# Kernel tuning notes

Measured on AMD Instinct MI355X. Metric: run time of the kernel, lower is better.

Reference implementation:

```python
import jax, jax.numpy as jnp
import numpy as np

B, F, U, H1, H2 = 2048, 256, 64, 64, 32
E = F + 1  # attention embed dim = num_inputs + 1


def setup_inputs() -> dict:
    key = jax.random.key(0)
    ks = jax.random.split(key, 14)
    s = lambda fan: 1.0 / np.sqrt(fan)
    inp = {
        "x": jax.random.normal(ks[0], (B, F), jnp.float32),
        # stacked per-feature FeatureNN params (Linear(1,U) -> Linear(U,H1) -> Linear(H1,H2) -> Linear(H2,1))
        "w1": jax.random.normal(ks[1], (F, U), jnp.float32) * s(1),
        "b1": jnp.zeros((F, U), jnp.float32),
        "w2": jax.random.normal(ks[2], (F, U, H1), jnp.float32) * s(U),
        "b2": jnp.zeros((F, H1), jnp.float32),
        "w3": jax.random.normal(ks[3], (F, H1, H2), jnp.float32) * s(H1),
        "b3": jnp.zeros((F, H2), jnp.float32),
        "w4": jax.random.normal(ks[4], (F, H2), jnp.float32) * s(H2),
        "b4": jnp.zeros((F,), jnp.float32),
        # MultiheadAttention(E, 1) params: packed qkv in_proj + out_proj
        "in_w": jax.random.normal(ks[5], (3 * E, E), jnp.float32) * s(E),
        "in_b": jnp.zeros((3 * E,), jnp.float32),
        "out_w": jax.random.normal(ks[6], (E, E), jnp.float32) * s(E),
        "out_b": jnp.zeros((E,), jnp.float32),
        "bias": jnp.zeros((1,), jnp.float32),
    }
    return inp


def _attention(x, in_w, in_b, out_w, out_b):
    # x: [B, F]; build [B, F, E] = concat(one-hot feature index, value)
    b = x.shape[0]
    eye = jnp.eye(F, dtype=x.dtype)
    xa = jnp.concatenate([jnp.broadcast_to(eye, (b, F, F)), x[:, :, None]], axis=-1)  # [B,F,E]
    qkv = jnp.einsum("bse,fe->bsf", xa, in_w) + in_b  # [B,F,3E]
    q, k, v = jnp.split(qkv, 3, axis=-1)
    scores = jnp.einsum("bqe,bke->bqk", q, k) / jnp.sqrt(jnp.asarray(E, x.dtype))
    attn = jax.nn.softmax(scores, axis=-1)
    ctx = jnp.einsum("bqk,bke->bqe", attn, v)
    out = jnp.einsum("bqe,fe->bqf", ctx, out_w) + out_b  # out_proj
    return out[:, :, -1]  # keep only the value channel -> [B, F]


def _feature_nns(x, w1, b1, w2, b2, w3, b3, w4, b4):
    # x: [B, F] -> per-feature independent MLPs, batched across features
    h = jax.nn.relu(x[:, :, None] * w1[None] + b1[None])          # [B,F,U]
    h = jax.nn.relu(jnp.einsum("bfu,fuh->bfh", h, w2) + b2[None])  # [B,F,H1]
    h = jax.nn.relu(jnp.einsum("bfh,fhg->bfg", h, w3) + b3[None])  # [B,F,H2]
    return jnp.einsum("bfg,fg->bf", h, w4) + b4[None]              # [B,F]


def reference(x, w1, b1, w2, b2, w3, b3, w4, b4, in_w, in_b, out_w, out_b, bias):
    xa = _attention(x, in_w, in_b, out_w, out_b)                   # att_before_flag=True
    fo = _feature_nns(xa, w1, b1, w2, b2, w3, b3, w4, b4)          # dropout is identity (p=0 / eval)
    out = jnp.sum(fo, axis=-1) + bias                              # [B] + bias -> [B]
    return (out, fo)
```

## Files before the change

### kernel.cpp

```cpp
#include <hip/hip_runtime.h>

#define BB 2048
#define FF 256
#define EE 257
#define UU 64
#define HH1 64
#define HH2 32

#define SC 0.089992807f

typedef __attribute__((ext_vector_type(8))) short short8;
typedef __attribute__((ext_vector_type(4))) float f32x4;
typedef __attribute__((ext_vector_type(4))) unsigned u32x4;
typedef __attribute__((ext_vector_type(2))) unsigned u32x2;

#define MF(a, b, c) __builtin_amdgcn_mfma_f32_16x16x32_bf16(a, b, c, 0, 0, 0)
#define EXP2(x) __builtin_amdgcn_exp2f(x)

__device__ inline unsigned cvt_pk(float a, float b) {
    unsigned r;
    asm("v_cvt_pk_bf16_f32 %0, %1, %2" : "=v"(r) : "v"(a), "v"(b));
    return r;
}
struct HiLo { unsigned hi, lo; };
__device__ inline HiLo split2(float a, float b) {
    HiLo r;
    r.hi = cvt_pk(a, b);
    float ha = __builtin_bit_cast(float, r.hi << 16);
    float hb = __builtin_bit_cast(float, r.hi & 0xFFFF0000u);
    r.lo = cvt_pk(a - ha, b - hb);
    return r;
}

__global__ __launch_bounds__(256) void k_prep(const float* __restrict__ in_w,
                                              const float* __restrict__ in_b,
                                              const float* __restrict__ out_w,
                                              const float* __restrict__ out_b,
                                              const float* __restrict__ w2,
                                              const float* __restrict__ w3,
                                              float* __restrict__ mt,
                                              float* __restrict__ uv, float* __restrict__ wgf,
                                              float* __restrict__ sc,
                                              short* __restrict__ w2s, short* __restrict__ w3s) {
    const int blk = blockIdx.x;
    const int t = threadIdx.x;
    __shared__ float red[4][256];
    __shared__ float s0[EE + 3];
    __shared__ float s1[EE + 3];
    if (blk < 256) {
        const int ki = blk;
        for (int j = t; j < EE; j += 256) {
            s0[j] = in_w[(EE + j) * EE + ki] + in_b[EE + j];
            s1[j] = in_b[j];
        }
        __syncthreads();
        const int w = t >> 6, l = t & 63;
        const int j0 = (w * EE) >> 2, j1 = ((w + 1) * EE) >> 2;
        float acc[4] = {0.f, 0.f, 0.f, 0.f};
#pragma unroll 4
        for (int j = j0; j < j1; ++j) {
            float ak = s0[j];
            float bj = s1[j];
#pragma unroll
            for (int g = 0; g < 4; ++g) {
                float aq = in_w[j * EE + l + 64 * g] + bj;
                acc[g] = fmaf(aq, ak, acc[g]);
            }
        }
#pragma unroll
        for (int g = 0; g < 4; ++g) red[w][l + 64 * g] = acc[g];
        __syncthreads();
        {
            float s = red[0][t] + red[1][t] + red[2][t] + red[3][t];
            mt[(ki >> 1) * 512 + t * 2 + (ki & 1)] = s * SC;
        }
    } else if (blk < 512) {
        const int f = blk - 256;
        const int l = t & 63, q = t >> 6;
        const int lr = l & 15, lq = l >> 4;
        const float* w2f = w2 + f * (UU * HH1);
        const float* w3f = w3 + f * (HH1 * HH2);
        short* o2 = w2s + f * 8192;
        short* o3 = w3s + f * 4096;
        const int hperm = (q & 1) * 32 + (lr >> 2) * 8 + ((q >> 1) << 2) + (lr & 3);
#pragma unroll
        for (int kb = 0; kb < 2; ++kb) {
            float v[8];
#pragma unroll
            for (int j = 0; j < 8; ++j) v[j] = w2f[(kb * 32 + lq * 8 + j) * HH1 + hperm];
            u32x4 hi, lo;
#pragma unroll
            for (int p = 0; p < 4; ++p) {
                HiLo s = split2(v[2 * p], v[2 * p + 1]);
                hi[p] = s.hi; lo[p] = s.lo;
            }
            *(short8*)(o2 + ((0 * 2 + kb) * 4 + q) * 512 + l * 8) = __builtin_bit_cast(short8, hi);
            *(short8*)(o2 + ((1 * 2 + kb) * 4 + q) * 512 + l * 8) = __builtin_bit_cast(short8, lo);
        }
        {
            const int kb = q & 1, ct = q >> 1;
            float v[8];
#pragma unroll
            for (int j = 0; j < 8; ++j) v[j] = w3f[(kb * 32 + lq * 8 + j) * HH2 + ct * 16 + lr];
            u32x4 hi, lo;
#pragma unroll
            for (int p = 0; p < 4; ++p) {
                HiLo s = split2(v[2 * p], v[2 * p + 1]);
                hi[p] = s.hi; lo[p] = s.lo;
            }
            *(short8*)(o3 + ((0 * 2 + kb) * 2 + ct) * 512 + l * 8) = __builtin_bit_cast(short8, hi);
            *(short8*)(o3 + ((1 * 2 + kb) * 2 + ct) * 512 + l * 8) = __builtin_bit_cast(short8, lo);
        }
    } else if (blk < 515) {
        const int which = blk - 512;
        for (int j = t; j < EE; j += 256) {
            if (which == 0)      { s0[j] = in_w[(EE + j) * EE + FF];    s1[j] = in_b[j]; }
            else if (which == 1) { s0[j] = in_w[j * EE + FF];           s1[j] = in_b[EE + j]; }
            else                 { s0[j] = out_w[(EE - 1) * EE + j];    s1[j] = in_b[2 * EE + j]; }
        }
        __syncthreads();
        const int w = t >> 6, l = t & 63;
        const int j0 = (w * EE) >> 2, j1 = ((w + 1) * EE) >> 2;
        const int rowbase = which * EE;
        float acc[4] = {0.f, 0.f, 0.f, 0.f};
#pragma unroll 4
        for (int j = j0; j < j1; ++j) {
            float sk = s0[j];
            float bj = s1[j];
#pragma unroll
            for (int g = 0; g < 4; ++g) {
                float av = in_w[(rowbase + j) * EE + l + 64 * g] + bj;
                acc[g] = fmaf(av, sk, acc[g]);
            }
        }
#pragma unroll
        for (int g = 0; g < 4; ++g) red[w][l + 64 * g] = acc[g];
        __syncthreads();
        {
            float s = red[0][t] + red[1][t] + red[2][t] + red[3][t];
            if (which == 0)      uv[t]          = s * SC;
            else if (which == 1) wgf[2 * t]     = s * SC;
            else                 wgf[2 * t + 1] = s;
        }
    } else {
        const int j = t;
        float cq = in_w[j * EE + FF];
        float ck = in_w[(EE + j) * EE + FF];
        float cv = in_w[(2 * EE + j) * EE + FF];
        float rj = out_w[(EE - 1) * EE + j];
        float pa = cq * ck, pb = cv * rj;
        if (t == 0) {
            const int j2 = 256;
            pa += in_w[j2 * EE + FF] * in_w[(EE + j2) * EE + FF];
            pb += in_w[(2 * EE + j2) * EE + FF] * out_w[(EE - 1) * EE + j2];
        }
#pragma unroll
        for (int o = 32; o > 0; o >>= 1) {
            pa += __shfl_down(pa, o, 64);
            pb += __shfl_down(pb, o, 64);
        }
        if ((t & 63) == 0) { red[0][t >> 6] = pa; red[1][t >> 6] = pb; }
        __syncthreads();
        if (t == 0) {
            pa = red[0][0] + red[0][1] + red[0][2] + red[0][3];
            pb = red[1][0] + red[1][1] + red[1][2] + red[1][3];
            sc[0] = pa * SC;
            sc[1] = pb;
            sc[2] = out_b[EE - 1];
        }
    }
}

__global__ __launch_bounds__(256) void k2_attn(const float* __restrict__ x,
                                               const float2* __restrict__ mt2,
                                               const float* __restrict__ uv,
                                               const float* __restrict__ wg,
                                               const float* __restrict__ sc,
                                               float* __restrict__ xa) {
    const int qi = threadIdx.x;
    const int b0 = blockIdx.x * 2;
    __shared__ __align__(16) float xs0[FF];
    __shared__ __align__(16) float xs1[FF];
    __shared__ __align__(16) float wgs[2 * FF];
    xs0[qi] = x[b0 * FF + qi];
    xs1[qi] = x[(b0 + 1) * FF + qi];
    *(float2*)&wgs[2 * qi] = *(const float2*)&wg[2 * qi];
    const float alpha_s = sc[0], beta = sc[1], ob = sc[2];
    const float uq = uv[qi];
    __syncthreads();
    const float xq0 = xs0[qi];
    const float xq1 = xs1[qi];
    const float a0 = fmaf(alpha_s, xq0, uq);
    const float a1 = fmaf(alpha_s, xq1, uq);
    float le0 = 0.f, le1 = 0.f, p0 = 0.f, p1 = 0.f, q0 = 0.f, q1 = 0.f;
#pragma unroll 8
    for (int kp = 0; kp < FF / 2; ++kp) {
        const float2 m   = mt2[kp * FF + qi];
        const f32x4 wgk  = *(const f32x4*)&wgs[4 * kp];
        const float2 xk0 = *(const float2*)&xs0[2 * kp];
        const float2 xk1 = *(const float2*)&xs1[2 * kp];
        float e;
        e = EXP2(fmaf(xk0.x, a0, fmaf(wgk[0], xq0, m.x))); le0 += e; p0 = fmaf(e, wgk[1], p0); q0 = fmaf(e, xk0.x, q0);
        e = EXP2(fmaf(xk0.y, a0, fmaf(wgk[2], xq0, m.y))); le0 += e; p0 = fmaf(e, wgk[3], p0); q0 = fmaf(e, xk0.y, q0);
        e = EXP2(fmaf(xk1.x, a1, fmaf(wgk[0], xq1, m.x))); le1 += e; p1 = fmaf(e, wgk[1], p1); q1 = fmaf(e, xk1.x, q1);
        e = EXP2(fmaf(xk1.y, a1, fmaf(wgk[2], xq1, m.y))); le1 += e; p1 = fmaf(e, wgk[3], p1); q1 = fmaf(e, xk1.y, q1);
    }
    xa[b0 * FF + qi]       = (p0 + beta * q0) / le0 + ob;
    xa[(b0 + 1) * FF + qi] = (p1 + beta * q1) / le1 + ob;
}

__global__ __launch_bounds__(256, 3) void k3_fnn(const float* xa_in,
                                                 const float* __restrict__ w1,
                                                 const float* __restrict__ b1,
                                                 const float* __restrict__ b2,
                                                 const float* __restrict__ b3,
                                                 const float* __restrict__ w4,
                                                 const float* __restrict__ b4,
                                                 const short* __restrict__ w2s,
                                                 const short* __restrict__ w3s,
                                                 float* fo) {
    const int fidx = blockIdx.x & 255;
    const int f   = ((fidx & 7) << 5) | (fidx >> 3);
    const int rq  = blockIdx.x >> 8;
    const int tid = threadIdx.x;
    const int wv  = tid >> 6;
    const int l   = tid & 63;
    const int lr  = l & 15;
    const int lq  = l >> 4;

    const float* w1f = w1 + f * UU;
    const float* b1f = b1 + f * UU;
    const float* b2f = b2 + f * HH1;
    const float* b3f = b3 + f * HH2;
    const float* w4f = w4 + f * HH2;
    const short* w2sf = w2s + f * 8192;
    const short* w3sf = w3s + f * 4096;
    const float b4v  = b4[f];

    short8 W3h[2][2], W3l[2][2];
#pragma unroll
    for (int ct = 0; ct < 2; ++ct)
#pragma unroll
        for (int kb = 0; kb < 2; ++kb) {
            W3h[ct][kb] = *(const short8*)(w3sf + ((0 * 2 + kb) * 2 + ct) * 512 + l * 8);
            W3l[ct][kb] = *(const short8*)(w3sf + ((1 * 2 + kb) * 2 + ct) * 512 + l * 8);
        }
    f32x4 B3v[2], W4v[2];
#pragma unroll
    for (int ct = 0; ct < 2; ++ct) {
        B3v[ct] = *(const f32x4*)(b3f + ct * 16 + lq * 4);
        W4v[ct] = *(const f32x4*)(w4f + ct * 16 + lq * 4);
    }

    __shared__ __align__(16) short w2l[8192];
#pragma unroll
    for (int i = 0; i < 4; ++i)
        *(short8*)(w2l + (tid * 4 + i) * 8) = *(const short8*)(w2sf + (tid * 4 + i) * 8);
    __syncthreads();

    const int cstart = (rq * 64) / 3;
    const int cend   = ((rq + 1) * 64) / 3;
    int ch = cstart + wv;
    if (ch >= cend) return;
    float xv0 = xa_in[(ch * 32 + lr) * FF + f];
    float xv1 = xa_in[(ch * 32 + 16 + lr) * FF + f];
    for (; ch < cend; ch += 4) {
        const int rows0 = ch * 32;
        float nxv0 = 0.f, nxv1 = 0.f;
        if (ch + 4 < cend) {
            nxv0 = xa_in[((ch + 4) * 32 + lr) * FF + f];
            nxv1 = xa_in[((ch + 4) * 32 + 16 + lr) * FF + f];
        }

        short8 Bh[2][2], Bl[2][2];
#pragma unroll
        for (int kb = 0; kb < 2; ++kb) {
            f32x4 wA = *(const f32x4*)(w1f + kb * 32 + lq * 8);
            f32x4 wB = *(const f32x4*)(w1f + kb * 32 + lq * 8 + 4);
            f32x4 bA = *(const f32x4*)(b1f + kb * 32 + lq * 8);
            f32x4 bB = *(const f32x4*)(b1f + kb * 32 + lq * 8 + 4);
#pragma unroll
            for (int rbt = 0; rbt < 2; ++rbt) {
                const float xv = rbt ? xv1 : xv0;
                float h[8];
#pragma unroll
                for (int j = 0; j < 4; ++j) h[j]     = fmaxf(fmaf(xv, wA[j], bA[j]), 0.f);
#pragma unroll
                for (int j = 0; j < 4; ++j) h[4 + j] = fmaxf(fmaf(xv, wB[j], bB[j]), 0.f);
                u32x4 bh, bl;
#pragma unroll
                for (int p = 0; p < 4; ++p) {
                    HiLo s = split2(h[2 * p], h[2 * p + 1]);
                    bh[p] = s.hi; bl[p] = s.lo;
                }
                Bh[rbt][kb] = __builtin_bit_cast(short8, bh);
                Bl[rbt][kb] = __builtin_bit_cast(short8, bl);
            }
        }

        f32x4 acc[2][4];
#pragma unroll
        for (int ht = 0; ht < 4; ++ht) {
            const short8 W2h0 = *(const short8*)(w2l + (0 * 4 + ht) * 512 + l * 8);
            const short8 W2h1 = *(const short8*)(w2l + (1 * 4 + ht) * 512 + l * 8);
            const short8 W2l0 = *(const short8*)(w2l + (2 * 4 + ht) * 512 + l * 8);
            const short8 W2l1 = *(const short8*)(w2l + (3 * 4 + ht) * 512 + l * 8);
            const f32x4 binit = *(const f32x4*)(b2f + (ht & 1) * 32 + lq * 8 + ((ht >> 1) << 2));
#pragma unroll
            for (int rbt = 0; rbt < 2; ++rbt) {
                f32x4 a = binit;
                a = MF(W2h0, Bh[rbt][0], a);
                a = MF(W2h1, Bh[rbt][1], a);
                a = MF(W2h0, Bl[rbt][0], a);
                a = MF(W2h1, Bl[rbt][1], a);
                a = MF(W2l0, Bh[rbt][0], a);
                a = MF(W2l1, Bh[rbt][1], a);
                acc[rbt][ht] = a;
            }
        }

#pragma unroll
        for (int rbt = 0; rbt < 2; ++rbt) {
            short8 Bh3[2], Bl3[2];
#pragma unroll
            for (int kb = 0; kb < 2; ++kb) {
                float e0 = fmaxf(acc[rbt][kb][0], 0.f),     e1 = fmaxf(acc[rbt][kb][1], 0.f);
                float e2 = fmaxf(acc[rbt][kb][2], 0.f),     e3 = fmaxf(acc[rbt][kb][3], 0.f);
                float e4 = fmaxf(acc[rbt][kb + 2][0], 0.f), e5 = fmaxf(acc[rbt][kb + 2][1], 0.f);
                float e6 = fmaxf(acc[rbt][kb + 2][2], 0.f), e7 = fmaxf(acc[rbt][kb + 2][3], 0.f);
                HiLo p0 = split2(e0, e1), p1 = split2(e2, e3);
                HiLo p2 = split2(e4, e5), p3 = split2(e6, e7);
                u32x4 bh, bl;
                bh[0] = p0.hi; bh[1] = p1.hi; bh[2] = p2.hi; bh[3] = p3.hi;
                bl[0] = p0.lo; bl[1] = p1.lo; bl[2] = p2.lo; bl[3] = p3.lo;
                Bh3[kb] = __builtin_bit_cast(short8, bh);
                Bl3[kb] = __builtin_bit_cast(short8, bl);
            }
            float part = 0.f;
#pragma unroll
            for (int ct = 0; ct < 2; ++ct) {
                f32x4 a2 = B3v[ct];
                a2 = MF(W3h[ct][0], Bh3[0], a2);
                a2 = MF(W3h[ct][1], Bh3[1], a2);
                a2 = MF(W3h[ct][0], Bl3[0], a2);
                a2 = MF(W3h[ct][1], Bl3[1], a2);
                a2 = MF(W3l[ct][0], Bh3[0], a2);
                a2 = MF(W3l[ct][1], Bh3[1], a2);
#pragma unroll
                for (int r = 0; r < 4; ++r)
                    part = fmaf(fmaxf(a2[r], 0.f), W4v[ct][r], part);
            }
            part += __shfl_xor(part, 16, 64);
            part += __shfl_xor(part, 32, 64);
            if (lq == 0)
                fo[(rows0 + rbt * 16 + lr) * FF + f] = part + b4v;
        }

        xv0 = nxv0; xv1 = nxv1;
    }
}

__global__ __launch_bounds__(64) void k4_sum(const float* __restrict__ fo,
                                             const float* __restrict__ bias,
                                             float* __restrict__ out) {
    const int b = blockIdx.x;
    const int t = threadIdx.x;
    const float* r = fo + b * FF;
    float s = r[t] + r[t + 64] + r[t + 128] + r[t + 192];
#pragma unroll
    for (int o = 32; o > 0; o >>= 1) s += __shfl_down(s, o, 64);
    if (t == 0) out[b] = s + bias[0];
}

extern "C" void kernel_launch(void* const* d_in, const int* in_sizes, int n_in,
                              void* d_out, int out_size, void* d_ws, size_t ws_size,
                              hipStream_t stream) {
    const float* x    = (const float*)d_in[0];
    const float* w1   = (const float*)d_in[1];
    const float* b1   = (const float*)d_in[2];
    const float* w2   = (const float*)d_in[3];
    const float* b2   = (const float*)d_in[4];
    const float* w3   = (const float*)d_in[5];
    const float* b3   = (const float*)d_in[6];
    const float* w4   = (const float*)d_in[7];
    const float* b4   = (const float*)d_in[8];
    const float* in_w = (const float*)d_in[9];
    const float* in_b = (const float*)d_in[10];
    const float* out_w= (const float*)d_in[11];
    const float* out_b= (const float*)d_in[12];
    const float* bias = (const float*)d_in[13];

    float* out = (float*)d_out;
    float* fo  = out + BB;
    float* ws  = (float*)d_ws;
    float* mt  = ws;
    float* uvp = ws + 65536;
    float* wgp = ws + 65792;
    float* scp = ws + 66304;
    short* w2s = (short*)(ws + 66560);
    short* w3s = w2s + 256 * 8192;

    k_prep<<<516, 256, 0, stream>>>(in_w, in_b, out_w, out_b, w2, w3,
                                    mt, uvp, wgp, scp, w2s, w3s);
    k2_attn<<<BB / 2, 256, 0, stream>>>(x, (const float2*)mt, uvp, wgp, scp, fo);
    k3_fnn<<<FF * 3, 256, 0, stream>>>(fo, w1, b1, b2, b3, w4, b4, w2s, w3s, fo);
    k4_sum<<<BB, 64, 0, stream>>>(fo, bias, out);
}
```

Before: 66.73 us.

## Split attention key loop across waves with LDS reduction; hoist FNN bias loads

The attention kernel now gives each wave a quarter of the key range while each lane handles four queries, instead of every thread looping over all 256 keys for one query. Partial softmax sums are combined through a shared-memory reduction after a barrier. This raises per-thread register use and adds LDS traffic and a sync, with the aim of reusing the per-key LDS loads across four queries. Separately, the layer-2 bias vectors in the FNN kernel are loaded once before the loop instead of on every chunk iteration.

```diff
diff --git a/kernel.cpp b/kernel.cpp
--- a/kernel.cpp
+++ b/kernel.cpp
@@ -177,36 +177,61 @@
                                                const float* __restrict__ wg,
                                                const float* __restrict__ sc,
                                                float* __restrict__ xa) {
-    const int qi = threadIdx.x;
+    const int t = threadIdx.x;
+    const int w = t >> 6, l = t & 63;
     const int b0 = blockIdx.x * 2;
     __shared__ __align__(16) float xs0[FF];
     __shared__ __align__(16) float xs1[FF];
     __shared__ __align__(16) float wgs[2 * FF];
-    xs0[qi] = x[b0 * FF + qi];
-    xs1[qi] = x[(b0 + 1) * FF + qi];
-    *(float2*)&wgs[2 * qi] = *(const float2*)&wg[2 * qi];
+    __shared__ float rr[6][4][256];
+    xs0[t] = x[b0 * FF + t];
+    xs1[t] = x[(b0 + 1) * FF + t];
+    *(float2*)&wgs[2 * t] = *(const float2*)&wg[2 * t];
     const float alpha_s = sc[0], beta = sc[1], ob = sc[2];
-    const float uq = uv[qi];
     __syncthreads();
-    const float xq0 = xs0[qi];
-    const float xq1 = xs1[qi];
-    const float a0 = fmaf(alpha_s, xq0, uq);
-    const float a1 = fmaf(alpha_s, xq1, uq);
-    float le0 = 0.f, le1 = 0.f, p0 = 0.f, p1 = 0.f, q0 = 0.f, q1 = 0.f;
-#pragma unroll 8
-    for (int kp = 0; kp < FF / 2; ++kp) {
-        const float2 m   = mt2[kp * FF + qi];
+    float xq0[4], xq1[4], A0[4], A1[4];
+#pragma unroll
+    for (int g = 0; g < 4; ++g) {
+        const int qi = l + 64 * g;
+        const float u = uv[qi];
+        xq0[g] = xs0[qi]; xq1[g] = xs1[qi];
+        A0[g] = fmaf(alpha_s, xq0[g], u);
+        A1[g] = fmaf(alpha_s, xq1[g], u);
+    }
+    float le0[4], le1[4], p0[4], p1[4], q0[4], q1[4];
+#pragma unroll
+    for (int g = 0; g < 4; ++g) { le0[g]=0.f; le1[g]=0.f; p0[g]=0.f; p1[g]=0.f; q0[g]=0.f; q1[g]=0.f; }
+    const int kp0 = w * 32;
+#pragma unroll 2
+    for (int kp = kp0; kp < kp0 + 32; ++kp) {
         const f32x4 wgk  = *(const f32x4*)&wgs[4 * kp];
         const float2 xk0 = *(const float2*)&xs0[2 * kp];
         const float2 xk1 = *(const float2*)&xs1[2 * kp];
-        float e;
-        e = EXP2(fmaf(xk0.x, a0, fmaf(wgk[0], xq0, m.x))); le0 += e; p0 = fmaf(e, wgk[1], p0); q0 = fmaf(e, xk0.x, q0);
-        e = EXP2(fmaf(xk0.y, a0, fmaf(wgk[2], xq0, m.y))); le0 += e; p0 = fmaf(e, wgk[3], p0); q0 = fmaf(e, xk0.y, q0);
-        e = EXP2(fmaf(xk1.x, a1, fmaf(wgk[0], xq1, m.x))); le1 += e; p1 = fmaf(e, wgk[1], p1); q1 = fmaf(e, xk1.x, q1);
-        e = EXP2(fmaf(xk1.y, a1, fmaf(wgk[2], xq1, m.y))); le1 += e; p1 = fmaf(e, wgk[3], p1); q1 = fmaf(e, xk1.y, q1);
-    }
-    xa[b0 * FF + qi]       = (p0 + beta * q0) / le0 + ob;
-    xa[(b0 + 1) * FF + qi] = (p1 + beta * q1) / le1 + ob;
+#pragma unroll
+        for (int g = 0; g < 4; ++g) {
+            const float2 m = mt2[kp * FF + l + 64 * g];
+            float e;
+            e = EXP2(fmaf(xk0.x, A0[g], fmaf(wgk[0], xq0[g], m.x))); le0[g] += e; p0[g] = fmaf(e, wgk[1], p0[g]); q0[g] = fmaf(e, xk0.x, q0[g]);
+            e = EXP2(fmaf(xk0.y, A0[g], fmaf(wgk[2], xq0[g], m.y))); le0[g] += e; p0[g] = fmaf(e, wgk[3], p0[g]); q0[g] = fmaf(e, xk0.y, q0[g]);
+            e = EXP2(fmaf(xk1.x, A1[g], fmaf(wgk[0], xq1[g], m.x))); le1[g] += e; p1[g] = fmaf(e, wgk[1], p1[g]); q1[g] = fmaf(e, xk1.x, q1[g]);
+            e = EXP2(fmaf(xk1.y, A1[g], fmaf(wgk[2], xq1[g], m.y))); le1[g] += e; p1[g] = fmaf(e, wgk[3], p1[g]); q1[g] = fmaf(e, xk1.y, q1[g]);
+        }
+    }
+#pragma unroll
+    for (int g = 0; g < 4; ++g) {
+        const int qi = l + 64 * g;
+        rr[0][w][qi] = le0[g]; rr[1][w][qi] = le1[g]; rr[2][w][qi] = p0[g];
+        rr[3][w][qi] = p1[g];  rr[4][w][qi] = q0[g];  rr[5][w][qi] = q1[g];
+    }
+    __syncthreads();
+    float LE0 = 0.f, LE1 = 0.f, P0 = 0.f, P1 = 0.f, Q0 = 0.f, Q1 = 0.f;
+#pragma unroll
+    for (int u2 = 0; u2 < 4; ++u2) {
+        LE0 += rr[0][u2][t]; LE1 += rr[1][u2][t]; P0 += rr[2][u2][t];
+        P1 += rr[3][u2][t];  Q0 += rr[4][u2][t];  Q1 += rr[5][u2][t];
+    }
+    xa[b0 * FF + t]       = (P0 + beta * Q0) / LE0 + ob;
+    xa[(b0 + 1) * FF + t] = (P1 + beta * Q1) / LE1 + ob;
 }
 
 __global__ __launch_bounds__(256, 3) void k3_fnn(const float* xa_in,
@@ -251,6 +276,10 @@
         B3v[ct] = *(const f32x4*)(b3f + ct * 16 + lq * 4);
         W4v[ct] = *(const f32x4*)(w4f + ct * 16 + lq * 4);
     }
+    f32x4 B2v[4];
+#pragma unroll
+    for (int ht = 0; ht < 4; ++ht)
+        B2v[ht] = *(const f32x4*)(b2f + (ht & 1) * 32 + lq * 8 + ((ht >> 1) << 2));
 
     __shared__ __align__(16) short w2l[8192];
 #pragma unroll
@@ -305,10 +334,9 @@
             const short8 W2h1 = *(const short8*)(w2l + (1 * 4 + ht) * 512 + l * 8);
             const short8 W2l0 = *(const short8*)(w2l + (2 * 4 + ht) * 512 + l * 8);
             const short8 W2l1 = *(const short8*)(w2l + (3 * 4 + ht) * 512 + l * 8);
-            const f32x4 binit = *(const f32x4*)(b2f + (ht & 1) * 32 + lq * 8 + ((ht >> 1) << 2));
 #pragma unroll
             for (int rbt = 0; rbt < 2; ++rbt) {
-                f32x4 a = binit;
+                f32x4 a = B2v[ht];
                 a = MF(W2h0, Bh[rbt][0], a);
                 a = MF(W2h1, Bh[rbt][1], a);
                 a = MF(W2h0, Bl[rbt][0], a);
```

After: 64.37 us (median of 2 runs). -3.5%, faster.
